# Performance work log

Measured on AMD Instinct MI355X. Metric: run time of the kernel, lower is better.

Reference implementation:

```python
import jax, jax.numpy as jnp
import numpy as np

T, B, H, E, V = 128, 64, 512, 256, 32000
UNK = 2
EPS = 1e-10


def setup_inputs() -> dict:
    key = jax.random.key(0)
    ks = jax.random.split(key, 16)
    s = 0.02
    return {
        "u_enc_out": jax.random.normal(ks[0], (T, B, H), jnp.float32),
        "z_tm1": jax.random.randint(ks[1], (1, B), 0, V),
        "last_hidden": jax.random.normal(ks[2], (1, B, H), jnp.float32),
        "u_input": jax.random.randint(ks[3], (T, B), 0, V),
        "emb": jax.random.normal(ks[4], (V, E), jnp.float32) * s,
        "attn_W": jax.random.normal(ks[5], (H, 2 * H), jnp.float32) * s,
        "attn_b": jnp.zeros((H,), jnp.float32),
        "attn_v": jax.random.normal(ks[6], (H,), jnp.float32) * (1.0 / np.sqrt(H)),
        "gru_Wih": jax.random.normal(ks[7], (3 * H, H + E), jnp.float32) * s,
        "gru_Whh": jax.random.normal(ks[8], (3 * H, H), jnp.float32) * s,
        "gru_bih": jnp.zeros((3 * H,), jnp.float32),
        "gru_bhh": jnp.zeros((3 * H,), jnp.float32),
        "proj_W": jax.random.normal(ks[9], (V, 2 * H), jnp.float32) * s,
        "proj_b": jnp.zeros((V,), jnp.float32),
        "copy1_W": jax.random.normal(ks[10], (H, H), jnp.float32) * s,
        "copy1_b": jnp.zeros((H,), jnp.float32),
    }


def _copy_logscore(raw, u_input):
    # raw: [B,T] copy scores; u_input: [T,B] int ids
    # Faithful to: log(bmm(exp(raw - max), sparse_one_hot_with_1e-10_floor)) + max
    cmax = jnp.max(raw, axis=1, keepdims=True)            # [B,1]
    ex = jnp.exp(raw - cmax)                              # [B,T]
    idx = u_input.T                                       # [B,T]
    idx = jnp.where(idx == UNK, V + jnp.arange(T)[None, :], idx)
    mask = (u_input.T != 0).astype(ex.dtype)
    total = jnp.sum(ex, axis=1)                           # [B] (all t, incl. ignored)
    scat = jax.vmap(lambda e, i: jnp.zeros((V + T,), ex.dtype).at[i].add(e))(ex * mask, idx)
    return jnp.log(EPS * total[:, None] + (1.0 - EPS) * scat) + cmax  # [B,V+T]


def reference(u_enc_out, z_tm1, last_hidden, u_input, emb, attn_W, attn_b, attn_v,
              gru_Wih, gru_Whh, gru_bih, gru_bhh, proj_W, proj_b, copy1_W, copy1_b):
    enc = jnp.transpose(u_enc_out, (1, 0, 2))             # [B,T,H]
    h = last_hidden[0]                                    # [B,H]
    # Attn: energy = tanh(Linear([h;enc])), score = v . energy, softmax over T
    Hrep = jnp.broadcast_to(h[:, None, :], enc.shape)
    energy = jnp.tanh(jnp.einsum('bti,hi->bth', jnp.concatenate([Hrep, enc], -1), attn_W) + attn_b)
    alpha = jax.nn.softmax(jnp.einsum('h,bth->bt', attn_v, energy), axis=1)
    ctx = jnp.einsum('bt,bth->bh', alpha, enc)            # [B,H]
    # GRU step (pytorch gate order r,z,n)
    x = jnp.concatenate([emb[z_tm1[0]], ctx], axis=-1)    # [B,E+H]
    gi = x @ gru_Wih.T + gru_bih
    gh = h @ gru_Whh.T + gru_bhh
    i_r, i_z, i_n = jnp.split(gi, 3, axis=-1)
    h_r, h_z, h_n = jnp.split(gh, 3, axis=-1)
    r = jax.nn.sigmoid(i_r + h_r)
    z = jax.nn.sigmoid(i_z + h_z)
    n = jnp.tanh(i_n + r * h_n)
    h_new = (1.0 - z) * n + z * h                         # [B,H]
    gru_out = h_new[None]                                 # [1,B,H]
    new_hidden = h_new[None]
    # generation score
    gen_score = jnp.concatenate([h_new, ctx], -1) @ proj_W.T + proj_b  # [B,V]
    # copy score
    cs = jnp.tanh(jnp.einsum('bth,ih->bti', enc, copy1_W) + copy1_b)   # [B,T,H]
    raw = jnp.einsum('bth,bh->bt', cs, h_new)             # [B,T]
    u_copy = _copy_logscore(raw, u_input)                 # [B,V+T]
    scores = jax.nn.softmax(jnp.concatenate([gen_score, u_copy], axis=1), axis=1)
    g, c = scores[:, :V], scores[:, V:]                   # [B,V], [B,V+T]
    proba = jnp.concatenate([g + c[:, :V], c[:, V:]], axis=1)  # [B,V+T]
    return gru_out, new_hidden, proba
```

## Files before the change

kernel.cpp:

```cpp
#include <hip/hip_runtime.h>
#include <math.h>

#define T_ 128
#define B_ 64
#define H_ 512
#define E_ 256
#define V_ 32000
#define VT_ (V_ + T_)
#define UNK_ 2
#define EPS_ 1e-10f
#define NS_ 16

typedef __attribute__((ext_vector_type(8))) __bf16 bf16x8;
typedef __attribute__((ext_vector_type(4))) float floatx4;

#define NB_ZERO 64
#define NB_CVTE 2048
#define NB_CVTA 512
#define NB_CVTC 512
#define NB_WH   8192
#define NB_GH   24576
#define NB_PRO  (NB_ZERO + NB_CVTE + NB_CVTA + NB_CVTC + NB_WH + NB_GH)

__global__ __launch_bounds__(256) void prologue_k(
        const float* __restrict__ u_enc, const float* __restrict__ attn_W,
        const float* __restrict__ copy1_W, const float* __restrict__ last_h,
        const float* __restrict__ attn_b, const float* __restrict__ gru_Whh,
        const float* __restrict__ gru_bhh,
        float* __restrict__ zbase, __bf16* __restrict__ enc_bf,
        __bf16* __restrict__ Wb_attn, __bf16* __restrict__ Wb_copy,
        float* __restrict__ Wh, float* __restrict__ gh) {
    int bid = blockIdx.x, tid = threadIdx.x;
    if (bid < NB_ZERO) { zbase[bid * 256 + tid] = 0.f; return; }
    bid -= NB_ZERO;
    if (bid < NB_CVTE) {
        int i = (bid * 256 + tid) * 8;
        float4 a = *(const float4*)(u_enc + i);
        float4 b = *(const float4*)(u_enc + i + 4);
        bf16x8 o;
        o[0] = (__bf16)a.x; o[1] = (__bf16)a.y; o[2] = (__bf16)a.z; o[3] = (__bf16)a.w;
        o[4] = (__bf16)b.x; o[5] = (__bf16)b.y; o[6] = (__bf16)b.z; o[7] = (__bf16)b.w;
        *(bf16x8*)(enc_bf + i) = o;
        return;
    }
    bid -= NB_CVTE;
    if (bid < NB_CVTA) {
        int c = tid * 2;
        float2 v = *(const float2*)(attn_W + (size_t)bid * 1024 + 512 + c);
        Wb_attn[bid * 512 + c]     = (__bf16)v.x;
        Wb_attn[bid * 512 + c + 1] = (__bf16)v.y;
        return;
    }
    bid -= NB_CVTA;
    if (bid < NB_CVTC) {
        int c = tid * 2;
        float2 v = *(const float2*)(copy1_W + (size_t)bid * 512 + c);
        Wb_copy[bid * 512 + c]     = (__bf16)v.x;
        Wb_copy[bid * 512 + c + 1] = (__bf16)v.y;
        return;
    }
    bid -= NB_CVTC;
    if (bid < NB_WH) {
        int wid = bid * 4 + (tid >> 6), lane = tid & 63;
        int b = wid >> 9, m = wid & 511;
        const float4* wr = (const float4*)(attn_W + (size_t)m * 1024);
        const float4* xr = (const float4*)(last_h + b * 512);
        float s = 0.f;
        #pragma unroll
        for (int i = 0; i < 2; ++i) {
            int k = lane + i * 64;
            float4 w = wr[k], x = xr[k];
            s += w.x * x.x + w.y * x.y + w.z * x.z + w.w * x.w;
        }
        #pragma unroll
        for (int off = 32; off > 0; off >>= 1) s += __shfl_down(s, off);
        if (lane == 0) Wh[b * 512 + m] = s + attn_b[m];
        return;
    }
    bid -= NB_WH;
    {
        int wid = bid * 4 + (tid >> 6), lane = tid & 63;
        int b = wid / 1536, m = wid % 1536;
        const float4* wr = (const float4*)(gru_Whh + (size_t)m * 512);
        const float4* xr = (const float4*)(last_h + b * 512);
        float s = 0.f;
        #pragma unroll
        for (int i = 0; i < 2; ++i) {
            int k = lane + i * 64;
            float4 w = wr[k], x = xr[k];
            s += w.x * x.x + w.y * x.y + w.z * x.z + w.w * x.w;
        }
        #pragma unroll
        for (int off = 32; off > 0; off >>= 1) s += __shfl_down(s, off);
        if (lane == 0) gh[b * 1536 + m] = s + gru_bhh[m];
    }
}

__global__ __launch_bounds__(256) void enc_mfma_dot_k(
        const __bf16* __restrict__ enc_bf,
        const __bf16* __restrict__ Wb,
        const float* __restrict__ addv, int add_per_b,
        const float* __restrict__ dotv, int dot_per_b,
        float* __restrict__ out) {
    int lane = threadIdx.x & 63;
    int wave = threadIdx.x >> 6;
    int r0 = blockIdx.x * 64;
    int b  = r0 / T_;
    int t0 = r0 % T_;
    int n0 = blockIdx.y * 64 + wave * 16;
    int coln = lane & 15;
    int kq   = (lane >> 4) * 8;
    const __bf16* wrow = Wb + (size_t)(n0 + coln) * H_ + kq;
    floatx4 acc[4] = {};
    #pragma unroll 4
    for (int k0 = 0; k0 < H_; k0 += 32) {
        bf16x8 fb = *(const bf16x8*)(wrow + k0);
        #pragma unroll
        for (int mi = 0; mi < 4; ++mi) {
            const __bf16* arow = enc_bf +
                ((size_t)(t0 + mi * 16 + coln) * B_ + b) * H_ + k0 + kq;
            bf16x8 fa = *(const bf16x8*)arow;
            acc[mi] = __builtin_amdgcn_mfma_f32_16x16x32_bf16(fa, fb, acc[mi], 0, 0, 0);
        }
    }
    int col = n0 + coln;
    float addt = add_per_b ? addv[b * H_ + col] : addv[col];
    float dt   = dot_per_b ? dotv[b * H_ + col] : dotv[col];
    int rbase = (lane >> 4) * 4;
    #pragma unroll
    for (int mi = 0; mi < 4; ++mi)
        #pragma unroll
        for (int r = 0; r < 4; ++r) {
            float x = acc[mi][r] + addt;
            float t = __expf(2.f * x);
            float v = dt * ((t - 1.f) / (t + 1.f));
            v += __shfl_xor(v, 1);
            v += __shfl_xor(v, 2);
            v += __shfl_xor(v, 4);
            v += __shfl_xor(v, 8);
            if (coln == 0) atomicAdd(&out[r0 + mi * 16 + rbase + r], v);
        }
}

__global__ void softmax_t_k(const float* __restrict__ score, float* __restrict__ alpha) {
    __shared__ float red[T_];
    int b = blockIdx.x, t = threadIdx.x;
    float v = score[b * T_ + t];
    red[t] = v; __syncthreads();
    for (int s = 64; s > 0; s >>= 1) { if (t < s) red[t] = fmaxf(red[t], red[t + s]); __syncthreads(); }
    float m = red[0]; __syncthreads();
    float e = __expf(v - m);
    red[t] = e; __syncthreads();
    for (int s = 64; s > 0; s >>= 1) { if (t < s) red[t] += red[t + s]; __syncthreads(); }
    alpha[b * T_ + t] = e / red[0];
}

__global__ void ctx_k(const float* __restrict__ enc, const float* __restrict__ alpha,
                      float* __restrict__ ctx, __bf16* __restrict__ xcat_bf) {
    __shared__ float al[T_];
    int b = blockIdx.x;
    int h = blockIdx.y * 256 + threadIdx.x;
    if (threadIdx.x < T_) al[threadIdx.x] = alpha[b * T_ + threadIdx.x];
    __syncthreads();
    float s = 0.f;
    for (int t = 0; t < T_; ++t) s += al[t] * enc[((size_t)t * B_ + b) * H_ + h];
    ctx[b * H_ + h] = s;
    xcat_bf[b * 1024 + 512 + h] = (__bf16)s;
}

__global__ void gi_matvec_k(const float* __restrict__ Wih,
                            const float* __restrict__ emb,
                            const int* __restrict__ z,
                            const float* __restrict__ ctx,
                            const float* __restrict__ bih,
                            float* __restrict__ gi) {
    const int M = 1536, K = 768;
    int wid  = blockIdx.x * 4 + (threadIdx.x >> 6);
    int lane = threadIdx.x & 63;
    int b = wid / M, m = wid % M;
    if (b >= B_) return;
    const float4* wr = (const float4*)(Wih + (size_t)m * K);
    const float4* er = (const float4*)(emb + (size_t)z[b] * E_);
    const float4* cr = (const float4*)(ctx + (size_t)b * H_);
    float s = 0.f;
    for (int k = lane; k < K / 4; k += 64) {
        float4 xv = (k < E_ / 4) ? er[k] : cr[k - E_ / 4];
        float4 w = wr[k];
        s += w.x * xv.x + w.y * xv.y + w.z * xv.z + w.w * xv.w;
    }
    #pragma unroll
    for (int off = 32; off > 0; off >>= 1) s += __shfl_down(s, off);
    if (lane == 0) gi[b * M + m] = s + bih[m];
}

__global__ void gru_k(const float* __restrict__ gi, const float* __restrict__ gh,
                      const float* __restrict__ hprev,
                      float* __restrict__ out, __bf16* __restrict__ xcat_bf) {
    int b = blockIdx.x;
    int m = blockIdx.y * 256 + threadIdx.x;
    float ir = gi[b * 1536 + m],        hr = gh[b * 1536 + m];
    float iz = gi[b * 1536 + 512 + m],  hz = gh[b * 1536 + 512 + m];
    float in_ = gi[b * 1536 + 1024 + m], hn = gh[b * 1536 + 1024 + m];
    float r = 1.f / (1.f + __expf(-(ir + hr)));
    float z = 1.f / (1.f + __expf(-(iz + hz)));
    float n = tanhf(in_ + r * hn);
    float h = hprev[b * 512 + m];
    float hv = (1.f - z) * n + z * h;
    out[b * 512 + m] = hv;
    out[B_ * 512 + b * 512 + m] = hv;
    xcat_bf[b * 1024 + m] = (__bf16)hv;
}

__global__ __launch_bounds__(256) void proj_mfma_k(
        const __bf16* __restrict__ xcat_bf,
        const float* __restrict__ Wp,
        const float* __restrict__ bp,
        float* __restrict__ gen) {
    int lane = threadIdx.x & 63;
    int wave = threadIdx.x >> 6;
    int n0 = (blockIdx.x * 4 + wave) * 16;
    int col = lane & 15;
    int kq  = (lane >> 4) * 8;
    const float* wrow = Wp + (size_t)(n0 + col) * 1024 + kq;
    const __bf16* abase = xcat_bf + kq;
    floatx4 acc[4] = {};
    #pragma unroll 8
    for (int k0 = 0; k0 < 1024; k0 += 32) {
        const float4* wb = (const float4*)(wrow + k0);
        float4 b0 = wb[0], b1 = wb[1];
        bf16x8 fb;
        fb[0] = (__bf16)b0.x; fb[1] = (__bf16)b0.y; fb[2] = (__bf16)b0.z; fb[3] = (__bf16)b0.w;
        fb[4] = (__bf16)b1.x; fb[5] = (__bf16)b1.y; fb[6] = (__bf16)b1.z; fb[7] = (__bf16)b1.w;
        #pragma unroll
        for (int mi = 0; mi < 4; ++mi) {
            bf16x8 fa = *(const bf16x8*)(abase + (size_t)(mi * 16 + col) * 1024 + k0);
            acc[mi] = __builtin_amdgcn_mfma_f32_16x16x32_bf16(fa, fb, acc[mi], 0, 0, 0);
        }
    }
    int rbase = (lane >> 4) * 4;
    float bias = bp[n0 + col];
    #pragma unroll
    for (int mi = 0; mi < 4; ++mi)
        #pragma unroll
        for (int r = 0; r < 4; ++r) {
            int b = mi * 16 + rbase + r;
            gen[(size_t)b * V_ + n0 + col] = acc[mi][r] + bias;
        }
}

__global__ void copy_epi_k(const float* __restrict__ raw,
                           const int* __restrict__ u_input,
                           float* __restrict__ scat, float* __restrict__ sc4) {
    __shared__ float red[T_];
    int b = blockIdx.x, t = threadIdx.x;
    float v = raw[b * T_ + t];
    red[t] = v; __syncthreads();
    for (int s = 64; s > 0; s >>= 1) { if (t < s) red[t] = fmaxf(red[t], red[t + s]); __syncthreads(); }
    float cm = red[0]; __syncthreads();
    float e = __expf(v - cm);
    red[t] = e; __syncthreads();
    for (int s = 64; s > 0; s >>= 1) { if (t < s) red[t] += red[t + s]; __syncthreads(); }
    float tot = red[0]; __syncthreads();
    int id = u_input[t * B_ + b];
    size_t j = (size_t)b * VT_ + ((id == UNK_) ? (V_ + t) : id);
    if (id != 0) scat[j] = 0.f;
    __syncthreads();
    if (id != 0) atomicAdd(&scat[j], e);
    red[t] = (id != 0) ? e : 0.f; __syncthreads();
    for (int s = 64; s > 0; s >>= 1) { if (t < s) red[t] += red[t + s]; __syncthreads(); }
    float ssum = red[0]; __syncthreads();
    float sv = (id != 0) ? scat[j] : 0.f;
    red[t] = sv; __syncthreads();
    for (int s = 64; s > 0; s >>= 1) { if (t < s) red[t] = fmaxf(red[t], red[t + s]); __syncthreads(); }
    if (t == 0) {
        sc4[b * 4 + 0] = cm;
        sc4[b * 4 + 1] = tot;
        sc4[b * 4 + 2] = ssum;
        sc4[b * 4 + 3] = red[0];
    }
}

__global__ __launch_bounds__(256) void gen_stats_k(const float* __restrict__ gen,
                                                   float* __restrict__ mpart,
                                                   float* __restrict__ lpart) {
    int b = blockIdx.x, s = blockIdx.y, tid = threadIdx.x;
    const int C = V_ / NS_;
    const float* gr = gen + (size_t)b * V_ + s * C;
    __shared__ float red[256];
    float m = -1e30f;
    for (int j = tid; j < C; j += 256) m = fmaxf(m, gr[j]);
    red[tid] = m; __syncthreads();
    for (int st = 128; st > 0; st >>= 1) { if (tid < st) red[tid] = fmaxf(red[tid], red[tid + st]); __syncthreads(); }
    m = red[0]; __syncthreads();
    float l = 0.f;
    for (int j = tid; j < C; j += 256) l += __expf(gr[j] - m);
    red[tid] = l; __syncthreads();
    for (int st = 128; st > 0; st >>= 1) { if (tid < st) red[tid] += red[tid + st]; __syncthreads(); }
    if (tid == 0) { mpart[b * NS_ + s] = m; lpart[b * NS_ + s] = red[0]; }
}

__global__ void combine2_k(const float* __restrict__ mpart, const float* __restrict__ lpart,
                           const float* __restrict__ sc4, float* __restrict__ params) {
    int b = threadIdx.x;
    float Mg = -1e30f;
    #pragma unroll
    for (int s = 0; s < NS_; s++) Mg = fmaxf(Mg, mpart[b * NS_ + s]);
    float cm = sc4[b * 4], tot = sc4[b * 4 + 1], ssum = sc4[b * 4 + 2], smax = sc4[b * 4 + 3];
    float umax = cm + logf(EPS_ * tot + (1.f - EPS_) * smax);
    float M = fmaxf(Mg, umax);
    float Zg = 0.f;
    #pragma unroll
    for (int s = 0; s < NS_; s++) Zg += lpart[b * NS_ + s] * __expf(mpart[b * NS_ + s] - M);
    float coef = __expf(cm - M);
    float Z = Zg + coef * (EPS_ * tot * (float)VT_ + (1.f - EPS_) * ssum);
    float invZ = 1.f / Z;
    params[b * 4 + 0] = M;
    params[b * 4 + 1] = invZ;
    params[b * 4 + 2] = coef * EPS_ * tot * invZ;
    params[b * 4 + 3] = coef * (1.f - EPS_) * invZ;
}

__global__ __launch_bounds__(256) void write_k(const float* __restrict__ gen,
                                               const float* __restrict__ params,
                                               float* __restrict__ proba) {
    int b = blockIdx.y;
    int i4 = blockIdx.x * 256 + threadIdx.x;
    if (i4 >= VT_ / 4) return;
    float M = params[b * 4], invZ = params[b * 4 + 1], addc = params[b * 4 + 2];
    int j = i4 * 4;
    float4 p;
    if (j < V_) {
        float4 g = *(const float4*)(gen + (size_t)b * V_ + j);
        p.x = addc + __expf(g.x - M) * invZ;
        p.y = addc + __expf(g.y - M) * invZ;
        p.z = addc + __expf(g.z - M) * invZ;
        p.w = addc + __expf(g.w - M) * invZ;
    } else {
        p.x = p.y = p.z = p.w = addc;
    }
    *(float4*)(proba + (size_t)b * VT_ + j) = p;
}

__global__ void fix_k(const float* __restrict__ gen, const float* __restrict__ scat,
                      const int* __restrict__ u_input, const float* __restrict__ params,
                      float* __restrict__ proba) {
    int b = blockIdx.x, t = threadIdx.x;
    int id = u_input[t * B_ + b];
    if (id == 0) return;
    int j = (id == UNK_) ? (V_ + t) : id;
    float M = params[b * 4], invZ = params[b * 4 + 1];
    float addc = params[b * 4 + 2], scoef = params[b * 4 + 3];
    float p = addc + scoef * scat[(size_t)b * VT_ + j];
    if (j < V_) p += __expf(gen[(size_t)b * V_ + j] - M) * invZ;
    proba[(size_t)b * VT_ + j] = p;
}

extern "C" void kernel_launch(void* const* d_in, const int* in_sizes, int n_in,
                              void* d_out, int out_size, void* d_ws, size_t ws_size,
                              hipStream_t stream) {
    const float* u_enc   = (const float*)d_in[0];
    const int*   z_tm1   = (const int*)d_in[1];
    const float* last_h  = (const float*)d_in[2];
    const int*   u_input = (const int*)d_in[3];
    const float* emb     = (const float*)d_in[4];
    const float* attn_W  = (const float*)d_in[5];
    const float* attn_b  = (const float*)d_in[6];
    const float* attn_v  = (const float*)d_in[7];
    const float* gru_Wih = (const float*)d_in[8];
    const float* gru_Whh = (const float*)d_in[9];
    const float* gru_bih = (const float*)d_in[10];
    const float* gru_bhh = (const float*)d_in[11];
    const float* proj_W  = (const float*)d_in[12];
    const float* proj_b  = (const float*)d_in[13];
    const float* copy1_W = (const float*)d_in[14];
    const float* copy1_b = (const float*)d_in[15];
    float* out = (float*)d_out;

    float* ws    = (float*)d_ws;
    float* score = ws;
    float* rawb  = score + B_ * T_;
    float* gen   = rawb + B_ * T_;
    float* scat  = gen + (size_t)B_ * V_;
    float* Wh    = scat + (size_t)B_ * VT_;
    float* gh    = Wh + B_ * H_;
    float* alpha = gh + B_ * 1536;
    float* ctx   = alpha + B_ * T_;
    float* gi    = ctx + B_ * H_;
    float* sc4   = gi + B_ * 1536;
    float* mpart = sc4 + B_ * 4;
    float* lpart = mpart + B_ * NS_;
    float* params= lpart + B_ * NS_;
    __bf16* xcat_bf = (__bf16*)(params + B_ * 4);
    __bf16* enc_bf  = xcat_bf + B_ * 1024;
    __bf16* Wb_attn = enc_bf + (size_t)T_ * B_ * H_;
    __bf16* Wb_copy = Wb_attn + H_ * H_;

    prologue_k<<<NB_PRO, 256, 0, stream>>>(u_enc, attn_W, copy1_W, last_h, attn_b,
                                           gru_Whh, gru_bhh,
                                           score, enc_bf, Wb_attn, Wb_copy, Wh, gh);

    dim3 g2(T_ * B_ / 64, H_ / 64);
    enc_mfma_dot_k<<<g2, 256, 0, stream>>>(enc_bf, Wb_attn, Wh, 1, attn_v, 0, score);

    softmax_t_k<<<B_, T_, 0, stream>>>(score, alpha);
    ctx_k<<<dim3(B_, 2), 256, 0, stream>>>(u_enc, alpha, ctx, xcat_bf);
    gi_matvec_k<<<B_ * 1536 / 4, 256, 0, stream>>>(gru_Wih, emb, z_tm1, ctx, gru_bih, gi);
    gru_k<<<dim3(B_, 2), 256, 0, stream>>>(gi, gh, last_h, out, xcat_bf);

    proj_mfma_k<<<V_ / 64, 256, 0, stream>>>(xcat_bf, proj_W, proj_b, gen);

    enc_mfma_dot_k<<<g2, 256, 0, stream>>>(enc_bf, Wb_copy, copy1_b, 0, out, 1, rawb);

    copy_epi_k<<<B_, T_, 0, stream>>>(rawb, u_input, scat, sc4);
    gen_stats_k<<<dim3(B_, NS_), 256, 0, stream>>>(gen, mpart, lpart);
    combine2_k<<<1, B_, 0, stream>>>(mpart, lpart, sc4, params);

    float* proba = out + 2 * B_ * H_;
    write_k<<<dim3((VT_ / 4 + 255) / 256, B_), 256, 0, stream>>>(gen, params, proba);
    fix_k<<<B_, T_, 0, stream>>>(gen, scat, u_input, params, proba);
}
```

Baseline: 421.2 us.

## Fuse attention and copy encoder GEMMs, batch GRU via MFMA, fuse stats

Switches the bf16 paths to fp16 and merges the attention-score and copy-score encoder GEMMs into one kernel that reads the encoder once, storing tanh copy activations in fp16. Softmax and context are fused into one kernel. The GRU input and hidden matvecs become a single MFMA GEMM over concatenated weights. Projection max/sum stats are computed in the projection epilogue, and the raw copy dot is folded into the copy epilogue. This cuts launches and redundant encoder reads, but adds weight conversion work to the prologue and a large fp16 intermediate for the copy scores.

```diff
diff --git a/kernel.cpp b/kernel.cpp
--- a/kernel.cpp
+++ b/kernel.cpp
@@ -9,27 +9,33 @@
 #define VT_ (V_ + T_)
 #define UNK_ 2
 #define EPS_ 1e-10f
-#define NS_ 16
-
-typedef __attribute__((ext_vector_type(8))) __bf16 bf16x8;
+#define NP_ (V_ / 64)
+
+typedef __attribute__((ext_vector_type(8))) _Float16 half8;
 typedef __attribute__((ext_vector_type(4))) float floatx4;
 
-#define NB_ZERO 64
+#define NB_ZERO 32
 #define NB_CVTE 2048
 #define NB_CVTA 512
 #define NB_CVTC 512
 #define NB_WH   8192
-#define NB_GH   24576
-#define NB_PRO  (NB_ZERO + NB_CVTE + NB_CVTA + NB_CVTC + NB_WH + NB_GH)
+#define NB_CVTW 2048
+#define NB_XE   64
+#define NB_XH   128
+#define NB_BC   8
+#define NB_PRO (NB_ZERO + NB_CVTE + NB_CVTA + NB_CVTC + NB_WH + NB_CVTW + NB_XE + NB_XH + NB_BC)
 
 __global__ __launch_bounds__(256) void prologue_k(
         const float* __restrict__ u_enc, const float* __restrict__ attn_W,
         const float* __restrict__ copy1_W, const float* __restrict__ last_h,
-        const float* __restrict__ attn_b, const float* __restrict__ gru_Whh,
-        const float* __restrict__ gru_bhh,
-        float* __restrict__ zbase, __bf16* __restrict__ enc_bf,
-        __bf16* __restrict__ Wb_attn, __bf16* __restrict__ Wb_copy,
-        float* __restrict__ Wh, float* __restrict__ gh) {
+        const float* __restrict__ attn_b, const float* __restrict__ emb,
+        const int* __restrict__ z, const float* __restrict__ Wih,
+        const float* __restrict__ Whh, const float* __restrict__ bih,
+        const float* __restrict__ bhh,
+        float* __restrict__ zbase, _Float16* __restrict__ enc_h,
+        _Float16* __restrict__ Wb_attn, _Float16* __restrict__ Wb_copy,
+        float* __restrict__ Wh, _Float16* __restrict__ Wcat,
+        _Float16* __restrict__ xg, float* __restrict__ bcat) {
     int bid = blockIdx.x, tid = threadIdx.x;
     if (bid < NB_ZERO) { zbase[bid * 256 + tid] = 0.f; return; }
     bid -= NB_ZERO;
@@ -37,26 +43,26 @@
         int i = (bid * 256 + tid) * 8;
         float4 a = *(const float4*)(u_enc + i);
         float4 b = *(const float4*)(u_enc + i + 4);
-        bf16x8 o;
-        o[0] = (__bf16)a.x; o[1] = (__bf16)a.y; o[2] = (__bf16)a.z; o[3] = (__bf16)a.w;
-        o[4] = (__bf16)b.x; o[5] = (__bf16)b.y; o[6] = (__bf16)b.z; o[7] = (__bf16)b.w;
-        *(bf16x8*)(enc_bf + i) = o;
+        half8 o;
+        o[0] = (_Float16)a.x; o[1] = (_Float16)a.y; o[2] = (_Float16)a.z; o[3] = (_Float16)a.w;
+        o[4] = (_Float16)b.x; o[5] = (_Float16)b.y; o[6] = (_Float16)b.z; o[7] = (_Float16)b.w;
+        *(half8*)(enc_h + i) = o;
         return;
     }
     bid -= NB_CVTE;
     if (bid < NB_CVTA) {
         int c = tid * 2;
         float2 v = *(const float2*)(attn_W + (size_t)bid * 1024 + 512 + c);
-        Wb_attn[bid * 512 + c]     = (__bf16)v.x;
-        Wb_attn[bid * 512 + c + 1] = (__bf16)v.y;
+        Wb_attn[bid * 512 + c]     = (_Float16)v.x;
+        Wb_attn[bid * 512 + c + 1] = (_Float16)v.y;
         return;
     }
     bid -= NB_CVTA;
     if (bid < NB_CVTC) {
         int c = tid * 2;
         float2 v = *(const float2*)(copy1_W + (size_t)bid * 512 + c);
-        Wb_copy[bid * 512 + c]     = (__bf16)v.x;
-        Wb_copy[bid * 512 + c + 1] = (__bf16)v.y;
+        Wb_copy[bid * 512 + c]     = (_Float16)v.x;
+        Wb_copy[bid * 512 + c + 1] = (_Float16)v.y;
         return;
     }
     bid -= NB_CVTC;
@@ -78,30 +84,54 @@
         return;
     }
     bid -= NB_WH;
+    if (bid < NB_CVTW) {
+        int m = bid;
+        #pragma unroll
+        for (int j = 0; j < 5; ++j) {
+            int c = j * 256 + tid;
+            float w;
+            if (m < 1024)      w = (c < 768) ? Wih[(size_t)m * 768 + c]
+                                             : Whh[(size_t)m * 512 + (c - 768)];
+            else if (m < 1536) w = (c < 768) ? Wih[(size_t)m * 768 + c] : 0.f;
+            else               w = (c >= 768) ? Whh[(size_t)(m - 512) * 512 + (c - 768)] : 0.f;
+            Wcat[(size_t)m * 1280 + c] = (_Float16)w;
+        }
+        return;
+    }
+    bid -= NB_CVTW;
+    if (bid < NB_XE) {
+        int idx = bid * 256 + tid;
+        int bb = idx >> 8, c = idx & 255;
+        xg[bb * 1280 + c] = (_Float16)emb[(size_t)z[bb] * E_ + c];
+        return;
+    }
+    bid -= NB_XE;
+    if (bid < NB_XH) {
+        int idx = bid * 256 + tid;
+        int bb = idx >> 9, c = idx & 511;
+        xg[bb * 1280 + 768 + c] = (_Float16)last_h[bb * H_ + c];
+        return;
+    }
+    bid -= NB_XH;
     {
-        int wid = bid * 4 + (tid >> 6), lane = tid & 63;
-        int b = wid / 1536, m = wid % 1536;
-        const float4* wr = (const float4*)(gru_Whh + (size_t)m * 512);
-        const float4* xr = (const float4*)(last_h + b * 512);
-        float s = 0.f;
-        #pragma unroll
-        for (int i = 0; i < 2; ++i) {
-            int k = lane + i * 64;
-            float4 w = wr[k], x = xr[k];
-            s += w.x * x.x + w.y * x.y + w.z * x.z + w.w * x.w;
-        }
-        #pragma unroll
-        for (int off = 32; off > 0; off >>= 1) s += __shfl_down(s, off);
-        if (lane == 0) gh[b * 1536 + m] = s + gru_bhh[m];
-    }
-}
-
-__global__ __launch_bounds__(256) void enc_mfma_dot_k(
-        const __bf16* __restrict__ enc_bf,
-        const __bf16* __restrict__ Wb,
-        const float* __restrict__ addv, int add_per_b,
-        const float* __restrict__ dotv, int dot_per_b,
-        float* __restrict__ out) {
+        int m = bid * 256 + tid;
+        float v2;
+        if (m < 1024)      v2 = bih[m] + bhh[m];
+        else if (m < 1536) v2 = bih[m];
+        else               v2 = bhh[m - 512];
+        bcat[m] = v2;
+    }
+}
+
+__global__ __launch_bounds__(256) void enc_dual_k(
+        const _Float16* __restrict__ enc_h,
+        const _Float16* __restrict__ Wa,
+        const _Float16* __restrict__ Wc,
+        const float* __restrict__ Wh,
+        const float* __restrict__ attn_v,
+        const float* __restrict__ copy1_b,
+        float* __restrict__ score,
+        _Float16* __restrict__ cs) {
     int lane = threadIdx.x & 63;
     int wave = threadIdx.x >> 6;
     int r0 = blockIdx.x * 64;
@@ -110,167 +140,226 @@
     int n0 = blockIdx.y * 64 + wave * 16;
     int coln = lane & 15;
     int kq   = (lane >> 4) * 8;
-    const __bf16* wrow = Wb + (size_t)(n0 + coln) * H_ + kq;
-    floatx4 acc[4] = {};
+    const _Float16* wra = Wa + (size_t)(n0 + coln) * H_ + kq;
+    const _Float16* wrc = Wc + (size_t)(n0 + coln) * H_ + kq;
+    floatx4 acca[4] = {}, accc[4] = {};
     #pragma unroll 4
     for (int k0 = 0; k0 < H_; k0 += 32) {
-        bf16x8 fb = *(const bf16x8*)(wrow + k0);
+        half8 fba = *(const half8*)(wra + k0);
+        half8 fbc = *(const half8*)(wrc + k0);
         #pragma unroll
         for (int mi = 0; mi < 4; ++mi) {
-            const __bf16* arow = enc_bf +
+            const _Float16* arow = enc_h +
                 ((size_t)(t0 + mi * 16 + coln) * B_ + b) * H_ + k0 + kq;
-            bf16x8 fa = *(const bf16x8*)arow;
-            acc[mi] = __builtin_amdgcn_mfma_f32_16x16x32_bf16(fa, fb, acc[mi], 0, 0, 0);
+            half8 fa = *(const half8*)arow;
+            acca[mi] = __builtin_amdgcn_mfma_f32_16x16x32_f16(fa, fba, acca[mi], 0, 0, 0);
+            accc[mi] = __builtin_amdgcn_mfma_f32_16x16x32_f16(fa, fbc, accc[mi], 0, 0, 0);
         }
     }
     int col = n0 + coln;
-    float addt = add_per_b ? addv[b * H_ + col] : addv[col];
-    float dt   = dot_per_b ? dotv[b * H_ + col] : dotv[col];
+    float addt = Wh[b * H_ + col];
+    float av   = attn_v[col];
+    float cb   = copy1_b[col];
     int rbase = (lane >> 4) * 4;
     #pragma unroll
     for (int mi = 0; mi < 4; ++mi)
         #pragma unroll
         for (int r = 0; r < 4; ++r) {
-            float x = acc[mi][r] + addt;
-            float t = __expf(2.f * x);
-            float v = dt * ((t - 1.f) / (t + 1.f));
+            int row = r0 + mi * 16 + rbase + r;
+            float x = acca[mi][r] + addt;
+            float t2 = __expf(2.f * x);
+            float v = av * ((t2 - 1.f) / (t2 + 1.f));
             v += __shfl_xor(v, 1);
             v += __shfl_xor(v, 2);
             v += __shfl_xor(v, 4);
             v += __shfl_xor(v, 8);
-            if (coln == 0) atomicAdd(&out[r0 + mi * 16 + rbase + r], v);
-        }
-}
-
-__global__ void softmax_t_k(const float* __restrict__ score, float* __restrict__ alpha) {
+            if (coln == 0) atomicAdd(&score[row], v);
+            float y = accc[mi][r] + cb;
+            float t3 = __expf(2.f * y);
+            cs[(size_t)row * H_ + col] = (_Float16)((t3 - 1.f) / (t3 + 1.f));
+        }
+}
+
+__global__ __launch_bounds__(256) void softctx_k(
+        const float* __restrict__ score, const float* __restrict__ u_enc,
+        _Float16* __restrict__ xcat, _Float16* __restrict__ xg) {
+    __shared__ float al[T_];
     __shared__ float red[T_];
-    int b = blockIdx.x, t = threadIdx.x;
-    float v = score[b * T_ + t];
-    red[t] = v; __syncthreads();
-    for (int s = 64; s > 0; s >>= 1) { if (t < s) red[t] = fmaxf(red[t], red[t + s]); __syncthreads(); }
+    int b = blockIdx.x, tid = threadIdx.x;
+    float v = (tid < T_) ? score[b * T_ + tid] : -1e30f;
+    if (tid < T_) red[tid] = v;
+    __syncthreads();
+    for (int s = 64; s > 0; s >>= 1) { if (tid < s) red[tid] = fmaxf(red[tid], red[tid + s]); __syncthreads(); }
     float m = red[0]; __syncthreads();
-    float e = __expf(v - m);
-    red[t] = e; __syncthreads();
-    for (int s = 64; s > 0; s >>= 1) { if (t < s) red[t] += red[t + s]; __syncthreads(); }
-    alpha[b * T_ + t] = e / red[0];
-}
-
-__global__ void ctx_k(const float* __restrict__ enc, const float* __restrict__ alpha,
-                      float* __restrict__ ctx, __bf16* __restrict__ xcat_bf) {
-    __shared__ float al[T_];
-    int b = blockIdx.x;
-    int h = blockIdx.y * 256 + threadIdx.x;
-    if (threadIdx.x < T_) al[threadIdx.x] = alpha[b * T_ + threadIdx.x];
-    __syncthreads();
-    float s = 0.f;
-    for (int t = 0; t < T_; ++t) s += al[t] * enc[((size_t)t * B_ + b) * H_ + h];
-    ctx[b * H_ + h] = s;
-    xcat_bf[b * 1024 + 512 + h] = (__bf16)s;
-}
-
-__global__ void gi_matvec_k(const float* __restrict__ Wih,
-                            const float* __restrict__ emb,
-                            const int* __restrict__ z,
-                            const float* __restrict__ ctx,
-                            const float* __restrict__ bih,
-                            float* __restrict__ gi) {
-    const int M = 1536, K = 768;
-    int wid  = blockIdx.x * 4 + (threadIdx.x >> 6);
-    int lane = threadIdx.x & 63;
-    int b = wid / M, m = wid % M;
-    if (b >= B_) return;
-    const float4* wr = (const float4*)(Wih + (size_t)m * K);
-    const float4* er = (const float4*)(emb + (size_t)z[b] * E_);
-    const float4* cr = (const float4*)(ctx + (size_t)b * H_);
-    float s = 0.f;
-    for (int k = lane; k < K / 4; k += 64) {
-        float4 xv = (k < E_ / 4) ? er[k] : cr[k - E_ / 4];
-        float4 w = wr[k];
-        s += w.x * xv.x + w.y * xv.y + w.z * xv.z + w.w * xv.w;
-    }
-    #pragma unroll
-    for (int off = 32; off > 0; off >>= 1) s += __shfl_down(s, off);
-    if (lane == 0) gi[b * M + m] = s + bih[m];
-}
-
-__global__ void gru_k(const float* __restrict__ gi, const float* __restrict__ gh,
-                      const float* __restrict__ hprev,
-                      float* __restrict__ out, __bf16* __restrict__ xcat_bf) {
-    int b = blockIdx.x;
-    int m = blockIdx.y * 256 + threadIdx.x;
-    float ir = gi[b * 1536 + m],        hr = gh[b * 1536 + m];
-    float iz = gi[b * 1536 + 512 + m],  hz = gh[b * 1536 + 512 + m];
-    float in_ = gi[b * 1536 + 1024 + m], hn = gh[b * 1536 + 1024 + m];
-    float r = 1.f / (1.f + __expf(-(ir + hr)));
-    float z = 1.f / (1.f + __expf(-(iz + hz)));
-    float n = tanhf(in_ + r * hn);
-    float h = hprev[b * 512 + m];
-    float hv = (1.f - z) * n + z * h;
-    out[b * 512 + m] = hv;
-    out[B_ * 512 + b * 512 + m] = hv;
-    xcat_bf[b * 1024 + m] = (__bf16)hv;
-}
-
-__global__ __launch_bounds__(256) void proj_mfma_k(
-        const __bf16* __restrict__ xcat_bf,
-        const float* __restrict__ Wp,
-        const float* __restrict__ bp,
-        float* __restrict__ gen) {
+    float e = (tid < T_) ? __expf(v - m) : 0.f;
+    if (tid < T_) red[tid] = e;
+    __syncthreads();
+    for (int s = 64; s > 0; s >>= 1) { if (tid < s) red[tid] += red[tid + s]; __syncthreads(); }
+    if (tid < T_) al[tid] = e / red[0];
+    __syncthreads();
+    int h = blockIdx.y * 256 + tid;
+    float s2 = 0.f;
+    #pragma unroll 4
+    for (int t = 0; t < T_; ++t) s2 += al[t] * u_enc[((size_t)t * B_ + b) * H_ + h];
+    xcat[b * 1024 + 512 + h] = (_Float16)s2;
+    xg[b * 1280 + 256 + h]   = (_Float16)s2;
+}
+
+__global__ __launch_bounds__(256) void grucat_k(
+        const _Float16* __restrict__ xg,
+        const _Float16* __restrict__ Wcat,
+        const float* __restrict__ bcat,
+        float* __restrict__ S) {
     int lane = threadIdx.x & 63;
     int wave = threadIdx.x >> 6;
     int n0 = (blockIdx.x * 4 + wave) * 16;
-    int col = lane & 15;
+    int coln = lane & 15;
     int kq  = (lane >> 4) * 8;
-    const float* wrow = Wp + (size_t)(n0 + col) * 1024 + kq;
-    const __bf16* abase = xcat_bf + kq;
+    const _Float16* wrow = Wcat + (size_t)(n0 + coln) * 1280 + kq;
+    const _Float16* abase = xg + kq;
+    floatx4 acc[4] = {};
+    #pragma unroll 8
+    for (int k0 = 0; k0 < 1280; k0 += 32) {
+        half8 fb = *(const half8*)(wrow + k0);
+        #pragma unroll
+        for (int mi = 0; mi < 4; ++mi) {
+            half8 fa = *(const half8*)(abase + (size_t)(mi * 16 + coln) * 1280 + k0);
+            acc[mi] = __builtin_amdgcn_mfma_f32_16x16x32_f16(fa, fb, acc[mi], 0, 0, 0);
+        }
+    }
+    int rbase = (lane >> 4) * 4;
+    float bias = bcat[n0 + coln];
+    #pragma unroll
+    for (int mi = 0; mi < 4; ++mi)
+        #pragma unroll
+        for (int r = 0; r < 4; ++r)
+            S[(size_t)(mi * 16 + rbase + r) * 2048 + n0 + coln] = acc[mi][r] + bias;
+}
+
+__global__ void gru_k(const float* __restrict__ S, const float* __restrict__ hprev,
+                      float* __restrict__ out, _Float16* __restrict__ xcat) {
+    int b = blockIdx.x;
+    int m = blockIdx.y * 256 + threadIdx.x;
+    float r  = 1.f / (1.f + __expf(-S[b * 2048 + m]));
+    float zz = 1.f / (1.f + __expf(-S[b * 2048 + 512 + m]));
+    float n  = tanhf(S[b * 2048 + 1024 + m] + r * S[b * 2048 + 1536 + m]);
+    float h = hprev[b * H_ + m];
+    float hv = (1.f - zz) * n + zz * h;
+    out[b * H_ + m] = hv;
+    out[B_ * H_ + b * H_ + m] = hv;
+    xcat[b * 1024 + m] = (_Float16)hv;
+}
+
+__global__ __launch_bounds__(256) void proj_stats_k(
+        const _Float16* __restrict__ xcat,
+        const float* __restrict__ Wp,
+        const float* __restrict__ bp,
+        float* __restrict__ gen,
+        float* __restrict__ mpart, float* __restrict__ lpart) {
+    __shared__ float m_lds[4][64];
+    __shared__ float l_lds[4][64];
+    int lane = threadIdx.x & 63;
+    int wave = threadIdx.x >> 6;
+    int n0 = (blockIdx.x * 4 + wave) * 16;
+    int coln = lane & 15;
+    int kq  = (lane >> 4) * 8;
+    const float* wrow = Wp + (size_t)(n0 + coln) * 1024 + kq;
+    const _Float16* abase = xcat + kq;
     floatx4 acc[4] = {};
     #pragma unroll 8
     for (int k0 = 0; k0 < 1024; k0 += 32) {
         const float4* wb = (const float4*)(wrow + k0);
-        float4 b0 = wb[0], b1 = wb[1];
-        bf16x8 fb;
-        fb[0] = (__bf16)b0.x; fb[1] = (__bf16)b0.y; fb[2] = (__bf16)b0.z; fb[3] = (__bf16)b0.w;
-        fb[4] = (__bf16)b1.x; fb[5] = (__bf16)b1.y; fb[6] = (__bf16)b1.z; fb[7] = (__bf16)b1.w;
+        float4 w0 = wb[0], w1 = wb[1];
+        half8 fb;
+        fb[0] = (_Float16)w0.x; fb[1] = (_Float16)w0.y; fb[2] = (_Float16)w0.z; fb[3] = (_Float16)w0.w;
+        fb[4] = (_Float16)w1.x; fb[5] = (_Float16)w1.y; fb[6] = (_Float16)w1.z; fb[7] = (_Float16)w1.w;
         #pragma unroll
         for (int mi = 0; mi < 4; ++mi) {
-            bf16x8 fa = *(const bf16x8*)(abase + (size_t)(mi * 16 + col) * 1024 + k0);
-            acc[mi] = __builtin_amdgcn_mfma_f32_16x16x32_bf16(fa, fb, acc[mi], 0, 0, 0);
+            half8 fa = *(const half8*)(abase + (size_t)(mi * 16 + coln) * 1024 + k0);
+            acc[mi] = __builtin_amdgcn_mfma_f32_16x16x32_f16(fa, fb, acc[mi], 0, 0, 0);
         }
     }
     int rbase = (lane >> 4) * 4;
-    float bias = bp[n0 + col];
+    float bias = bp[n0 + coln];
     #pragma unroll
     for (int mi = 0; mi < 4; ++mi)
         #pragma unroll
         for (int r = 0; r < 4; ++r) {
-            int b = mi * 16 + rbase + r;
-            gen[(size_t)b * V_ + n0 + col] = acc[mi][r] + bias;
-        }
-}
-
-__global__ void copy_epi_k(const float* __restrict__ raw,
-                           const int* __restrict__ u_input,
-                           float* __restrict__ scat, float* __restrict__ sc4) {
+            int brow = mi * 16 + rbase + r;
+            float x = acc[mi][r] + bias;
+            gen[(size_t)brow * V_ + n0 + coln] = x;
+            float mm = x;
+            mm = fmaxf(mm, __shfl_xor(mm, 1));
+            mm = fmaxf(mm, __shfl_xor(mm, 2));
+            mm = fmaxf(mm, __shfl_xor(mm, 4));
+            mm = fmaxf(mm, __shfl_xor(mm, 8));
+            float e = __expf(x - mm);
+            e += __shfl_xor(e, 1);
+            e += __shfl_xor(e, 2);
+            e += __shfl_xor(e, 4);
+            e += __shfl_xor(e, 8);
+            if (coln == 0) { m_lds[wave][brow] = mm; l_lds[wave][brow] = e; }
+        }
+    __syncthreads();
+    if (threadIdx.x < 64) {
+        int bb = threadIdx.x;
+        float M = m_lds[0][bb], L = l_lds[0][bb];
+        #pragma unroll
+        for (int w = 1; w < 4; ++w) {
+            float m2 = m_lds[w][bb], l2 = l_lds[w][bb];
+            float nm = fmaxf(M, m2);
+            L = L * __expf(M - nm) + l2 * __expf(m2 - nm);
+            M = nm;
+        }
+        mpart[bb * NP_ + blockIdx.x] = M;
+        lpart[bb * NP_ + blockIdx.x] = L;
+    }
+}
+
+__global__ __launch_bounds__(256) void raw_epi_k(
+        const _Float16* __restrict__ cs, const float* __restrict__ hnew,
+        const int* __restrict__ u_input, float* __restrict__ scat,
+        float* __restrict__ sc4) {
+    __shared__ float rawS[T_];
     __shared__ float red[T_];
-    int b = blockIdx.x, t = threadIdx.x;
-    float v = raw[b * T_ + t];
-    red[t] = v; __syncthreads();
+    int b = blockIdx.x, tid = threadIdx.x;
+    int lane = tid & 63, wave = tid >> 6;
+    const float4* hp = (const float4*)(hnew + b * H_ + lane * 8);
+    float4 ha = hp[0], hb = hp[1];
+    #pragma unroll 4
+    for (int i = 0; i < 32; ++i) {
+        int t = wave * 32 + i;
+        half8 c8 = *(const half8*)(cs + (size_t)(b * T_ + t) * H_ + lane * 8);
+        float s = (float)c8[0] * ha.x + (float)c8[1] * ha.y + (float)c8[2] * ha.z + (float)c8[3] * ha.w
+                + (float)c8[4] * hb.x + (float)c8[5] * hb.y + (float)c8[6] * hb.z + (float)c8[7] * hb.w;
+        #pragma unroll
+        for (int off = 32; off > 0; off >>= 1) s += __shfl_down(s, off);
+        if (lane == 0) rawS[t] = s;
+    }
+    __syncthreads();
+    int t = tid;
+    float v = (t < T_) ? rawS[t] : -1e30f;
+    if (t < T_) red[t] = v;
+    __syncthreads();
     for (int s = 64; s > 0; s >>= 1) { if (t < s) red[t] = fmaxf(red[t], red[t + s]); __syncthreads(); }
     float cm = red[0]; __syncthreads();
-    float e = __expf(v - cm);
-    red[t] = e; __syncthreads();
+    float e = (t < T_) ? __expf(v - cm) : 0.f;
+    if (t < T_) red[t] = e;
+    __syncthreads();
     for (int s = 64; s > 0; s >>= 1) { if (t < s) red[t] += red[t + s]; __syncthreads(); }
     float tot = red[0]; __syncthreads();
-    int id = u_input[t * B_ + b];
+    int id = (t < T_) ? u_input[t * B_ + b] : 0;
     size_t j = (size_t)b * VT_ + ((id == UNK_) ? (V_ + t) : id);
     if (id != 0) scat[j] = 0.f;
     __syncthreads();
     if (id != 0) atomicAdd(&scat[j], e);
-    red[t] = (id != 0) ? e : 0.f; __syncthreads();
+    if (t < T_) red[t] = (id != 0) ? e : 0.f;
+    __syncthreads();
     for (int s = 64; s > 0; s >>= 1) { if (t < s) red[t] += red[t + s]; __syncthreads(); }
     float ssum = red[0]; __syncthreads();
     float sv = (id != 0) ? scat[j] : 0.f;
-    red[t] = sv; __syncthreads();
+    if (t < T_) red[t] = sv;
+    __syncthreads();
     for (int s = 64; s > 0; s >>= 1) { if (t < s) red[t] = fmaxf(red[t], red[t + s]); __syncthreads(); }
     if (t == 0) {
         sc4[b * 4 + 0] = cm;
@@ -280,44 +369,41 @@
     }
 }
 
-__global__ __launch_bounds__(256) void gen_stats_k(const float* __restrict__ gen,
-                                                   float* __restrict__ mpart,
-                                                   float* __restrict__ lpart) {
-    int b = blockIdx.x, s = blockIdx.y, tid = threadIdx.x;
-    const int C = V_ / NS_;
-    const float* gr = gen + (size_t)b * V_ + s * C;
-    __shared__ float red[256];
-    float m = -1e30f;
-    for (int j = tid; j < C; j += 256) m = fmaxf(m, gr[j]);
-    red[tid] = m; __syncthreads();
-    for (int st = 128; st > 0; st >>= 1) { if (tid < st) red[tid] = fmaxf(red[tid], red[tid + st]); __syncthreads(); }
-    m = red[0]; __syncthreads();
-    float l = 0.f;
-    for (int j = tid; j < C; j += 256) l += __expf(gr[j] - m);
-    red[tid] = l; __syncthreads();
-    for (int st = 128; st > 0; st >>= 1) { if (tid < st) red[tid] += red[tid + st]; __syncthreads(); }
-    if (tid == 0) { mpart[b * NS_ + s] = m; lpart[b * NS_ + s] = red[0]; }
-}
-
-__global__ void combine2_k(const float* __restrict__ mpart, const float* __restrict__ lpart,
-                           const float* __restrict__ sc4, float* __restrict__ params) {
-    int b = threadIdx.x;
-    float Mg = -1e30f;
-    #pragma unroll
-    for (int s = 0; s < NS_; s++) Mg = fmaxf(Mg, mpart[b * NS_ + s]);
-    float cm = sc4[b * 4], tot = sc4[b * 4 + 1], ssum = sc4[b * 4 + 2], smax = sc4[b * 4 + 3];
-    float umax = cm + logf(EPS_ * tot + (1.f - EPS_) * smax);
-    float M = fmaxf(Mg, umax);
-    float Zg = 0.f;
-    #pragma unroll
-    for (int s = 0; s < NS_; s++) Zg += lpart[b * NS_ + s] * __expf(mpart[b * NS_ + s] - M);
-    float coef = __expf(cm - M);
-    float Z = Zg + coef * (EPS_ * tot * (float)VT_ + (1.f - EPS_) * ssum);
-    float invZ = 1.f / Z;
-    params[b * 4 + 0] = M;
-    params[b * 4 + 1] = invZ;
-    params[b * 4 + 2] = coef * EPS_ * tot * invZ;
-    params[b * 4 + 3] = coef * (1.f - EPS_) * invZ;
+__global__ void combine_k(const float* __restrict__ mpart, const float* __restrict__ lpart,
+                          const float* __restrict__ sc4, float* __restrict__ params) {
+    __shared__ float ms[256], ls[256];
+    int b = blockIdx.x, tid = threadIdx.x;
+    float M = -1e30f, L = 0.f;
+    for (int s = tid; s < NP_; s += 256) {
+        float m2 = mpart[b * NP_ + s], l2 = lpart[b * NP_ + s];
+        float nm = fmaxf(M, m2);
+        L = L * __expf(M - nm) + l2 * __expf(m2 - nm);
+        M = nm;
+    }
+    ms[tid] = M; ls[tid] = L;
+    __syncthreads();
+    for (int s = 128; s > 0; s >>= 1) {
+        if (tid < s) {
+            float m2 = ms[tid + s], l2 = ls[tid + s];
+            float nm = fmaxf(ms[tid], m2);
+            ls[tid] = ls[tid] * __expf(ms[tid] - nm) + l2 * __expf(m2 - nm);
+            ms[tid] = nm;
+        }
+        __syncthreads();
+    }
+    if (tid == 0) {
+        float Mg = ms[0], Zg = ls[0];
+        float cm = sc4[b * 4], tot = sc4[b * 4 + 1], ssum = sc4[b * 4 + 2], smax = sc4[b * 4 + 3];
+        float umax = cm + logf(EPS_ * tot + (1.f - EPS_) * smax);
+        float M2 = fmaxf(Mg, umax);
+        float coef = __expf(cm - M2);
+        float Z = Zg * __expf(Mg - M2) + coef * (EPS_ * tot * (float)VT_ + (1.f - EPS_) * ssum);
+        float invZ = 1.f / Z;
+        params[b * 4 + 0] = M2;
+        params[b * 4 + 1] = invZ;
+        params[b * 4 + 2] = coef * EPS_ * tot * invZ;
+        params[b * 4 + 3] = coef * (1.f - EPS_) * invZ;
+    }
 }
 
 __global__ __launch_bounds__(256) void write_k(const float* __restrict__ gen,
@@ -378,42 +464,42 @@
 
     float* ws    = (float*)d_ws;
     float* score = ws;
-    float* rawb  = score + B_ * T_;
-    float* gen   = rawb + B_ * T_;
+    float* gen   = score + B_ * T_;
     float* scat  = gen + (size_t)B_ * V_;
     float* Wh    = scat + (size_t)B_ * VT_;
-    float* gh    = Wh + B_ * H_;
-    float* alpha = gh + B_ * 1536;
-    float* ctx   = alpha + B_ * T_;
-    float* gi    = ctx + B_ * H_;
-    float* sc4   = gi + B_ * 1536;
+    float* S     = Wh + B_ * H_;
+    float* sc4   = S + B_ * 2048;
     float* mpart = sc4 + B_ * 4;
-    float* lpart = mpart + B_ * NS_;
-    float* params= lpart + B_ * NS_;
-    __bf16* xcat_bf = (__bf16*)(params + B_ * 4);
-    __bf16* enc_bf  = xcat_bf + B_ * 1024;
-    __bf16* Wb_attn = enc_bf + (size_t)T_ * B_ * H_;
-    __bf16* Wb_copy = Wb_attn + H_ * H_;
+    float* lpart = mpart + B_ * NP_;
+    float* params= lpart + B_ * NP_;
+    float* bcat  = params + B_ * 4;
+    _Float16* xcat  = (_Float16*)(bcat + 2048);
+    _Float16* xg    = xcat + B_ * 1024;
+    _Float16* enc_h = xg + B_ * 1280;
+    _Float16* Wb_attn = enc_h + (size_t)T_ * B_ * H_;
+    _Float16* Wb_copy = Wb_attn + H_ * H_;
+    _Float16* Wcat  = Wb_copy + H_ * H_;
+    _Float16* cs    = Wcat + 2048 * 1280;
 
     prologue_k<<<NB_PRO, 256, 0, stream>>>(u_enc, attn_W, copy1_W, last_h, attn_b,
-                                           gru_Whh, gru_bhh,
-                                           score, enc_bf, Wb_attn, Wb_copy, Wh, gh);
+                                           emb, z_tm1, gru_Wih, gru_Whh, gru_bih, gru_bhh,
+                                           score, enc_h, Wb_attn, Wb_copy, Wh, Wcat, xg, bcat);
 
     dim3 g2(T_ * B_ / 64, H_ / 64);
-    enc_mfma_dot_k<<<g2, 256, 0, stream>>>(enc_bf, Wb_attn, Wh, 1, attn_v, 0, score);
-
-    softmax_t_k<<<B_, T_, 0, stream>>>(score, alpha);
-    ctx_k<<<dim3(B_, 2), 256, 0, stream>>>(u_enc, alpha, ctx, xcat_bf);
-    gi_matvec_k<<<B_ * 1536 / 4, 256, 0, stream>>>(gru_Wih, emb, z_tm1, ctx, gru_bih, gi);
-    gru_k<<<dim3(B_, 2), 256, 0, stream>>>(gi, gh, last_h, out, xcat_bf);
-
-    proj_mfma_k<<<V_ / 64, 256, 0, stream>>>(xcat_bf, proj_W, proj_b, gen);
-
-    enc_mfma_dot_k<<<g2, 256, 0, stream>>>(enc_bf, Wb_copy, copy1_b, 0, out, 1, rawb);
-
-    copy_epi_k<<<B_, T_, 0, stream>>>(rawb, u_input, scat, sc4);
-    gen_stats_k<<<dim3(B_, NS_), 256, 0, stream>>>(gen, mpart, lpart);
-    combine2_k<<<1, B_, 0, stream>>>(mpart, lpart, sc4, params);
+    enc_dual_k<<<g2, 256, 0, stream>>>(enc_h, Wb_attn, Wb_copy, Wh, attn_v, copy1_b,
+                                       score, cs);
+
+    softctx_k<<<dim3(B_, 2), 256, 0, stream>>>(score, u_enc, xcat, xg);
+
+    grucat_k<<<2048 / 64, 256, 0, stream>>>(xg, Wcat, bcat, S);
+
+    gru_k<<<dim3(B_, 2), 256, 0, stream>>>(S, last_h, out, xcat);
+
+    proj_stats_k<<<NP_, 256, 0, stream>>>(xcat, proj_W, proj_b, gen, mpart, lpart);
+
+    raw_epi_k<<<B_, 256, 0, stream>>>(cs, out, u_input, scat, sc4);
+
+    combine_k<<<B_, 256, 0, stream>>>(mpart, lpart, sc4, params);
 
     float* proba = out + 2 * B_ * H_;
     write_k<<<dim3((VT_ / 4 + 255) / 256, B_), 256, 0, stream>>>(gen, params, proba);
```

New measurement: 395.9 us. 6.0% less time.
